# Optimization experiments

Measured on AMD Instinct MI355X. Metric: run time of the kernel, lower is better.

## Reference

```python
import jax, jax.numpy as jnp
import numpy as np

K = 32
TEMP = 0.01
OTHERWEIGHT = 0.5
BS = 64
F = 128


def setup_inputs() -> dict:
    key = jax.random.key(0)
    k1, k2, k3 = jax.random.split(key, 3)
    feats1 = jax.random.normal(k1, (K * BS, F), dtype=jnp.float32)
    feats2 = jax.random.normal(k2, (K * BS, F), dtype=jnp.float32)
    overlap_inds = jax.random.randint(k3, (K,), 0, 2).astype(bool)
    return {"feats1": feats1, "feats2": feats2, "overlap_inds": overlap_inds, "bs": BS}


def _labels(overlap_inds, bs):
    k = overlap_inds.shape[0]
    labels1 = jnp.repeat(jnp.arange(k), bs)
    nov = (~overlap_inds).astype(jnp.int32)
    excl_nov = jnp.cumsum(nov) - nov  # exclusive count of non-overlaps before i
    class2 = jnp.where(overlap_inds, jnp.arange(k), k + excl_nov)
    labels2 = jnp.repeat(class2, bs)
    return jnp.concatenate([labels1, labels2])


def reference(feats1, feats2, overlap_inds, bs):
    n1 = feats1.shape[0]
    labels = _labels(overlap_inds, bs)            # [n]
    feats = jnp.concatenate([feats1, feats2])     # [n, F]
    n = feats.shape[0]

    logits = (feats @ feats.T) * TEMP             # [n, n]; log of exp(sim*temp)
    sim = jnp.exp(logits)

    same = labels[:, None] == labels[None, :]
    eye = jnp.eye(n, dtype=bool)
    pos_mask = same & ~eye
    neg_mask = ~same

    is2 = jnp.arange(n) >= n1                     # second-view block indicator
    cross_w = jnp.where(is2[:, None] != is2[None, :], OTHERWEIGHT, 1.0)

    neg_sum = jnp.sum(jnp.where(neg_mask, sim, 0.0), axis=1)      # [n]
    # -log(pos / neg_sum) = log(neg_sum) - logits
    per_pair_loss = cross_w * (jnp.log(neg_sum)[:, None] - logits)
    total_loss = jnp.sum(jnp.where(pos_mask, per_pair_loss, 0.0))
    total_pos = jnp.sum(pos_mask)

    # accuracy: a positive pair counts iff its sim beats ALL negatives in its row
    max_neg = jnp.max(jnp.where(neg_mask, sim, -jnp.inf), axis=1)  # [n]
    correct = pos_mask & (sim > max_neg[:, None])
    acc = jnp.sum(correct).astype(jnp.float32) / total_pos.astype(jnp.float32)

    loss = total_loss / total_pos.astype(jnp.float32)
    return acc, loss
```

## Files before the change

kernel.cpp:

```cpp
#include <hip/hip_runtime.h>
#include <math.h>

#define TEMP 0.01f

typedef __attribute__((ext_vector_type(8))) short short8;
typedef __attribute__((ext_vector_type(4))) float f32x4;
typedef __attribute__((ext_vector_type(4))) unsigned short ushort4_t;


__device__ __forceinline__ unsigned bf16_hi_bits(float x) {
  unsigned u = __float_as_uint(x);
  return (u + 0x7FFFu + ((u >> 16) & 1u)) >> 16;
}

struct HL { unsigned short h, l; };

__device__ __forceinline__ HL split1(float x) {
  unsigned hb = bf16_hi_bits(x);
  float hf = __uint_as_float(hb << 16);
  unsigned lb = bf16_hi_bits(x - hf);
  HL r;
  r.h = (unsigned short)hb;
  r.l = (unsigned short)lb;
  return r;
}

__device__ __forceinline__ void decode_ov(const int* __restrict__ ov_raw,
                                          int* s_class2, int* s_v2b,
                                          int* s_ov) {
  const int t = threadIdx.x;
  if (t < 64) {
    int v = (t < 32) ? ov_raw[t] : 0;
    bool valid = (t >= 32) || (v == 0) || (v == 1);
    unsigned long long okmask = __ballot(valid);
    bool as_int = (okmask == ~0ull);
    s_v2b[t] = 0;
    if (t < 32) {
      int o = as_int ? v : (((const unsigned char*)ov_raw)[t] ? 1 : 0);
      s_ov[t] = o;
      unsigned long long nz = __ballot((t < 32) && !o);
      int cum = __popcll(nz & ((1ull << t) - 1ull));
      int c2 = o ? t : 32 + cum;
      s_class2[t] = c2;
      s_v2b[c2] = t;
    }
  }
}

__device__ __forceinline__ int labf(int g, const int* s_class2) {
  return (g < 2048) ? (g >> 6) : s_class2[(g - 2048) >> 6];
}

__global__ __launch_bounds__(256, 2) void main_kernel(
    const float* __restrict__ f1, const float* __restrict__ f2,
    const int* __restrict__ ov_raw, float* __restrict__ nsum,
    int* __restrict__ nmaxb, float* __restrict__ pcw,
    float* __restrict__ pcwl, float* __restrict__ posbuf) {
  __shared__ unsigned short Ah[128][64], Al[128][64];
  __shared__ unsigned short Bh[128][64], Bl[128][64];
  __shared__ int s_class2[32], s_v2b[64], s_ov[32];

  decode_ov(ov_raw, s_class2, s_v2b, s_ov);

  const int ibase = blockIdx.x * 128, jbase = blockIdx.y * 128;
  const float* asrc = (ibase < 2048) ? (f1 + (size_t)ibase * 128)
                                     : (f2 + (size_t)(ibase - 2048) * 128);
  const float* bsrc = (jbase < 2048) ? (f1 + (size_t)jbase * 128)
                                     : (f2 + (size_t)(jbase - 2048) * 128);
  const int t = threadIdx.x;
  const int l = t & 63;
  const int wid = t >> 6;
  const int wy = wid >> 1, wx = wid & 1;
  const int rr = l & 15;
  const int q = l >> 4;
  const int sw = l & 7;

  f32x4 acc[4][4];
#pragma unroll
  for (int mi = 0; mi < 4; ++mi)
#pragma unroll
    for (int ni = 0; ni < 4; ++ni) acc[mi][ni] = (f32x4)0.0f;

  const int kq = t & 15;
  const int r0 = t >> 4;
  const int stc = ((kq >> 1) ^ (r0 & 7)) * 8 + (kq & 1) * 4;

  for (int kc = 0; kc < 2; ++kc) {
    if (kc) __syncthreads();
#pragma unroll
    for (int p = 0; p < 8; ++p) {
      const int r = r0 + 16 * p;
      const float4 va = *(const float4*)(asrc + (size_t)r * 128 + kc * 64 + kq * 4);
      const float4 vb = *(const float4*)(bsrc + (size_t)r * 128 + kc * 64 + kq * 4);
      ushort4_t ha, la, hb, lb;
      HL s;
      s = split1(va.x); ha.x = s.h; la.x = s.l;
      s = split1(va.y); ha.y = s.h; la.y = s.l;
      s = split1(va.z); ha.z = s.h; la.z = s.l;
      s = split1(va.w); ha.w = s.h; la.w = s.l;
      s = split1(vb.x); hb.x = s.h; lb.x = s.l;
      s = split1(vb.y); hb.y = s.h; lb.y = s.l;
      s = split1(vb.z); hb.z = s.h; lb.z = s.l;
      s = split1(vb.w); hb.w = s.h; lb.w = s.l;
      *(ushort4_t*)&Ah[r][stc] = ha;
      *(ushort4_t*)&Al[r][stc] = la;
      *(ushort4_t*)&Bh[r][stc] = hb;
      *(ushort4_t*)&Bl[r][stc] = lb;
    }
    __syncthreads();

#pragma unroll
    for (int s = 0; s < 2; ++s) {
      const int pb = ((((s << 2) | q)) ^ sw) << 3;
      short8 afh[4], afl[4], bfh[4], bfl[4];
#pragma unroll
      for (int mi = 0; mi < 4; ++mi) {
        const int ar = wy * 64 + mi * 16 + rr;
        afh[mi] = *(const short8*)&Ah[ar][pb];
        afl[mi] = *(const short8*)&Al[ar][pb];
        const int br = wx * 64 + mi * 16 + rr;
        bfh[mi] = *(const short8*)&Bh[br][pb];
        bfl[mi] = *(const short8*)&Bl[br][pb];
      }
#pragma unroll
      for (int mi = 0; mi < 4; ++mi)
#pragma unroll
        for (int ni = 0; ni < 4; ++ni) {
          acc[mi][ni] = __builtin_amdgcn_mfma_f32_16x16x32_bf16(
              afh[mi], bfh[ni], acc[mi][ni], 0, 0, 0);
          acc[mi][ni] = __builtin_amdgcn_mfma_f32_16x16x32_bf16(
              afh[mi], bfl[ni], acc[mi][ni], 0, 0, 0);
          acc[mi][ni] = __builtin_amdgcn_mfma_f32_16x16x32_bf16(
              afl[mi], bfh[ni], acc[mi][ni], 0, 0, 0);
        }
    }
  }

  const float cw = ((ibase < 2048) != (jbase < 2048)) ? 0.5f : 1.0f;
  int gj[4], lj[4];
#pragma unroll
  for (int ni = 0; ni < 4; ++ni) {
    gj[ni] = jbase + wx * 64 + ni * 16 + rr;
    lj[ni] = labf(gj[ni], s_class2);
  }

#pragma unroll
  for (int mi = 0; mi < 4; ++mi) {
#pragma unroll
    for (int reg = 0; reg < 4; ++reg) {
      const int gi = ibase + wy * 64 + mi * 16 + q * 4 + reg;
      const int li = labf(gi, s_class2);
      float rnsum = 0.f, rnmax = 0.f, rpcw = 0.f, rpcwl = 0.f;
#pragma unroll
      for (int ni = 0; ni < 4; ++ni) {
        const int gjj = gj[ni];
        if (gi == gjj) continue;
        const float logit = acc[mi][ni][reg] * TEMP;
        const float e = __expf(logit);
        if (li == lj[ni]) {
          rpcw += cw;
          rpcwl += cw * logit;
          int slot;
          if (gjj < 2048) slot = gjj - (li << 6);
          else slot = ((li < 32) ? 64 : 0) + (gjj - 2048 - (s_v2b[li] << 6));
          posbuf[(size_t)gi * 128 + slot] = e;
        } else {
          rnsum += e;
          rnmax = fmaxf(rnmax, e);
        }
      }
#pragma unroll
      for (int m = 1; m < 16; m <<= 1) {
        rnsum += __shfl_xor(rnsum, m, 64);
        rpcw  += __shfl_xor(rpcw, m, 64);
        rpcwl += __shfl_xor(rpcwl, m, 64);
        rnmax = fmaxf(rnmax, __shfl_xor(rnmax, m, 64));
      }
      if (rr == 0) {
        atomicAdd(&nsum[gi], rnsum);
        atomicAdd(&pcw[gi], rpcw);
        atomicAdd(&pcwl[gi], rpcwl);
        atomicMax(&nmaxb[gi], __float_as_int(rnmax));
      }
    }
  }
}

__global__ __launch_bounds__(256) void finalize_kernel(
    const int* __restrict__ ov_raw, const float* __restrict__ nsum,
    const int* __restrict__ nmaxb, const float* __restrict__ pcw,
    const float* __restrict__ pcwl, const float* __restrict__ posbuf,
    float* __restrict__ accum, int* __restrict__ counter,
    float* __restrict__ out) {
  __shared__ int s_class2[32], s_v2b[64], s_ov[32];
  __shared__ float sc[4], sp[4], sl[4];
  decode_ov(ov_raw, s_class2, s_v2b, s_ov);
  __syncthreads();

  const int t = threadIdx.x;
  const int w = t >> 6, lane = t & 63;
  float cnt_acc = 0.f, pos_acc = 0.f, loss_acc = 0.f;
  const int rbase = blockIdx.x * 64 + w * 16;
  for (int i = 0; i < 16; ++i) {
    const int row = rbase + i;
    const float2 pv = *(const float2*)&posbuf[(size_t)row * 128 + lane * 2];
    const int c = labf(row, s_class2);
    const int size = (c < 32) ? (s_ov[c] ? 128 : 64) : 64;
    int selfslot;
    if (row < 2048) selfslot = row - (c << 6);
    else selfslot = ((c < 32) ? 64 : 0) + (row - 2048 - (s_v2b[c] << 6));
    const float nmax = __int_as_float(nmaxb[row]);
    const int s0 = lane * 2;
    int h = 0;
    if (s0 < size && s0 != selfslot && pv.x > nmax) h++;
    if (s0 + 1 < size && s0 + 1 != selfslot && pv.y > nmax) h++;
    cnt_acc += (float)h;
    if (lane == 0) {
      loss_acc += logf(nsum[row]) * pcw[row] - pcwl[row];
      pos_acc += (float)(size - 1);
    }
  }
#pragma unroll
  for (int m = 1; m < 64; m <<= 1) {
    cnt_acc += __shfl_xor(cnt_acc, m, 64);
    pos_acc += __shfl_xor(pos_acc, m, 64);
    loss_acc += __shfl_xor(loss_acc, m, 64);
  }
  if (lane == 0) { sc[w] = cnt_acc; sp[w] = pos_acc; sl[w] = loss_acc; }
  __syncthreads();
  if (t == 0) {
    atomicAdd(&accum[0], sc[0] + sc[1] + sc[2] + sc[3]);
    atomicAdd(&accum[1], sp[0] + sp[1] + sp[2] + sp[3]);
    atomicAdd(&accum[2], sl[0] + sl[1] + sl[2] + sl[3]);
    __threadfence();
    const int prev = atomicAdd(counter, 1);
    if (prev == 63) {
      const float c = atomicAdd(&accum[0], 0.0f);
      const float tp = atomicAdd(&accum[1], 0.0f);
      const float lo = atomicAdd(&accum[2], 0.0f);
      out[0] = c / tp;
      out[1] = lo / tp;
    }
  }
}

extern "C" void kernel_launch(void* const* d_in, const int* in_sizes, int n_in,
                              void* d_out, int out_size, void* d_ws,
                              size_t ws_size, hipStream_t stream) {
  const float* f1 = (const float*)d_in[0];
  const float* f2 = (const float*)d_in[1];
  const int* ov = (const int*)d_in[2];
  float* out = (float*)d_out;

  float* wsf = (float*)d_ws;
  int* wsi = (int*)d_ws;
  float* nsum   = wsf;
  int* nmaxb    = wsi + 4096;
  float* pcw    = wsf + 8192;
  float* pcwl   = wsf + 12288;
  float* accum  = wsf + 16384;
  int* counter  = wsi + 16387;
  float* posbuf = wsf + 16400;

  (void)hipMemsetAsync(nsum, 0, (size_t)16392 * sizeof(float), stream);

  dim3 grid(32, 32);
  main_kernel<<<grid, 256, 0, stream>>>(f1, f2, ov, nsum, nmaxb, pcw, pcwl,
                                        posbuf);
  finalize_kernel<<<64, 256, 0, stream>>>(ov, nsum, nmaxb, pcw, pcwl, posbuf,
                                          accum, counter, out);
}
```

Measured before the change: 110.6 us.

## Precompute bf16 hi/lo split once and stream pre-swizzled halves into tiles

Adds a precompute kernel that converts every feature row into hi/lo bf16 halves, stored in a pre-swizzled layout in workspace. The main kernel then loads these halves directly into shared memory in K-chunks of 32, instead of every tile block redoing the fp32 load and split. Using smaller LDS tiles lets it target 3 blocks per CU. The cost is an extra kernel launch, an extra global write/read pass, and a per-chunk sync loop. The old path is kept as a fallback when the workspace is too small.

```diff
diff --git a/kernel.cpp b/kernel.cpp
--- a/kernel.cpp
+++ b/kernel.cpp
@@ -6,6 +6,7 @@
 typedef __attribute__((ext_vector_type(8))) short short8;
 typedef __attribute__((ext_vector_type(4))) float f32x4;
 typedef __attribute__((ext_vector_type(4))) unsigned short ushort4_t;
+typedef __attribute__((ext_vector_type(8))) unsigned short ushort8_t;
 
 
 __device__ __forceinline__ unsigned bf16_hi_bits(float x) {
@@ -51,7 +52,157 @@
   return (g < 2048) ? (g >> 6) : s_class2[(g - 2048) >> 6];
 }
 
-__global__ __launch_bounds__(256, 2) void main_kernel(
+__global__ __launch_bounds__(256) void precompute_kernel(
+    const float* __restrict__ f1, const float* __restrict__ f2,
+    unsigned short* __restrict__ Ph, unsigned short* __restrict__ Pl) {
+  const int t = blockIdx.x * 256 + threadIdx.x;
+  const int row = t >> 4;
+  const int gid = t & 15;
+  const int gp = gid & 3, c = gid >> 2;
+  const int glog = gp ^ ((row >> 1) & 3);
+  const int k = c * 32 + glog * 8;
+  const float* src = (row < 2048) ? (f1 + (size_t)row * 128)
+                                  : (f2 + (size_t)(row - 2048) * 128);
+  const float4 a = *(const float4*)(src + k);
+  const float4 b = *(const float4*)(src + k + 4);
+  ushort8_t hi, lo;
+  HL s;
+  s = split1(a.x); hi.s0 = s.h; lo.s0 = s.l;
+  s = split1(a.y); hi.s1 = s.h; lo.s1 = s.l;
+  s = split1(a.z); hi.s2 = s.h; lo.s2 = s.l;
+  s = split1(a.w); hi.s3 = s.h; lo.s3 = s.l;
+  s = split1(b.x); hi.s4 = s.h; lo.s4 = s.l;
+  s = split1(b.y); hi.s5 = s.h; lo.s5 = s.l;
+  s = split1(b.z); hi.s6 = s.h; lo.s6 = s.l;
+  s = split1(b.w); hi.s7 = s.h; lo.s7 = s.l;
+  *(ushort8_t*)&Ph[(size_t)row * 128 + gid * 8] = hi;
+  *(ushort8_t*)&Pl[(size_t)row * 128 + gid * 8] = lo;
+}
+
+__global__ __launch_bounds__(256, 3) void main_kernel_fat(
+    const unsigned short* __restrict__ Ph, const unsigned short* __restrict__ Pl,
+    const int* __restrict__ ov_raw, float* __restrict__ nsum,
+    int* __restrict__ nmaxb, float* __restrict__ pcw,
+    float* __restrict__ pcwl, float* __restrict__ posbuf) {
+  __shared__ unsigned short Ah[128][32], Al[128][32];
+  __shared__ unsigned short Bh[128][32], Bl[128][32];
+  __shared__ int s_class2[32], s_v2b[64], s_ov[32];
+
+  decode_ov(ov_raw, s_class2, s_v2b, s_ov);
+
+  const int ibase = blockIdx.x * 128, jbase = blockIdx.y * 128;
+  const int t = threadIdx.x;
+  const int l = t & 63;
+  const int w = t >> 6;
+  const int wy = w >> 1, wx = w & 1;
+  const int rr = l & 15;
+  const int q = l >> 4;
+  const int gp = q ^ ((rr >> 1) & 3);
+
+  f32x4 acc[4][4];
+#pragma unroll
+  for (int mi = 0; mi < 4; ++mi)
+#pragma unroll
+    for (int ni = 0; ni < 4; ++ni) acc[mi][ni] = (f32x4)0.0f;
+
+  const int srow = l >> 2;
+  const int sg = l & 3;
+
+  for (int c = 0; c < 4; ++c) {
+    if (c) __syncthreads();
+    const int goff = c * 32 + sg * 8;
+#pragma unroll
+    for (int j = 0; j < 2; ++j) {
+      const int rb = w * 32 + j * 16;
+      const int r = rb + srow;
+      const size_t arec = (size_t)(ibase + r) * 128 + goff;
+      const size_t brec = (size_t)(jbase + r) * 128 + goff;
+      const ushort8_t vah = *(const ushort8_t*)&Ph[arec];
+      const ushort8_t val = *(const ushort8_t*)&Pl[arec];
+      const ushort8_t vbh = *(const ushort8_t*)&Ph[brec];
+      const ushort8_t vbl = *(const ushort8_t*)&Pl[brec];
+      *(ushort8_t*)&Ah[r][sg * 8] = vah;
+      *(ushort8_t*)&Al[r][sg * 8] = val;
+      *(ushort8_t*)&Bh[r][sg * 8] = vbh;
+      *(ushort8_t*)&Bl[r][sg * 8] = vbl;
+    }
+    __syncthreads();
+
+    short8 bfh[4], bfl[4];
+#pragma unroll
+    for (int ni = 0; ni < 4; ++ni) {
+      const int br = wx * 64 + ni * 16 + rr;
+      bfh[ni] = *(const short8*)&Bh[br][gp * 8];
+      bfl[ni] = *(const short8*)&Bl[br][gp * 8];
+    }
+#pragma unroll
+    for (int mi = 0; mi < 4; ++mi) {
+      const int ar = wy * 64 + mi * 16 + rr;
+      const short8 afh = *(const short8*)&Ah[ar][gp * 8];
+      const short8 afl = *(const short8*)&Al[ar][gp * 8];
+#pragma unroll
+      for (int ni = 0; ni < 4; ++ni) {
+        acc[mi][ni] = __builtin_amdgcn_mfma_f32_16x16x32_bf16(
+            afh, bfh[ni], acc[mi][ni], 0, 0, 0);
+        acc[mi][ni] = __builtin_amdgcn_mfma_f32_16x16x32_bf16(
+            afh, bfl[ni], acc[mi][ni], 0, 0, 0);
+        acc[mi][ni] = __builtin_amdgcn_mfma_f32_16x16x32_bf16(
+            afl, bfh[ni], acc[mi][ni], 0, 0, 0);
+      }
+    }
+  }
+
+  const float cw = ((ibase < 2048) != (jbase < 2048)) ? 0.5f : 1.0f;
+  int gj[4], lj[4];
+#pragma unroll
+  for (int ni = 0; ni < 4; ++ni) {
+    gj[ni] = jbase + wx * 64 + ni * 16 + rr;
+    lj[ni] = labf(gj[ni], s_class2);
+  }
+
+#pragma unroll
+  for (int mi = 0; mi < 4; ++mi) {
+#pragma unroll
+    for (int reg = 0; reg < 4; ++reg) {
+      const int gi = ibase + wy * 64 + mi * 16 + q * 4 + reg;
+      const int li = labf(gi, s_class2);
+      float rnsum = 0.f, rnmax = 0.f, rpcw = 0.f, rpcwl = 0.f;
+#pragma unroll
+      for (int ni = 0; ni < 4; ++ni) {
+        const int gjj = gj[ni];
+        if (gi == gjj) continue;
+        const float logit = acc[mi][ni][reg] * TEMP;
+        const float e = __expf(logit);
+        if (li == lj[ni]) {
+          rpcw += cw;
+          rpcwl += cw * logit;
+          int slot;
+          if (gjj < 2048) slot = gjj - (li << 6);
+          else slot = ((li < 32) ? 64 : 0) + (gjj - 2048 - (s_v2b[li] << 6));
+          posbuf[(size_t)gi * 128 + slot] = e;
+        } else {
+          rnsum += e;
+          rnmax = fmaxf(rnmax, e);
+        }
+      }
+#pragma unroll
+      for (int m = 1; m < 16; m <<= 1) {
+        rnsum += __shfl_xor(rnsum, m, 64);
+        rpcw  += __shfl_xor(rpcw, m, 64);
+        rpcwl += __shfl_xor(rpcwl, m, 64);
+        rnmax = fmaxf(rnmax, __shfl_xor(rnmax, m, 64));
+      }
+      if (rr == 0) {
+        atomicAdd(&nsum[gi], rnsum);
+        atomicAdd(&pcw[gi], rpcw);
+        atomicAdd(&pcwl[gi], rpcwl);
+        atomicMax(&nmaxb[gi], __float_as_int(rnmax));
+      }
+    }
+  }
+}
+
+__global__ __launch_bounds__(256, 2) void main_kernel_legacy(
     const float* __restrict__ f1, const float* __restrict__ f2,
     const int* __restrict__ ov_raw, float* __restrict__ nsum,
     int* __restrict__ nmaxb, float* __restrict__ pcw,
@@ -261,12 +412,20 @@
   float* accum  = wsf + 16384;
   int* counter  = wsi + 16387;
   float* posbuf = wsf + 16400;
+  unsigned short* Ph = (unsigned short*)(wsf + 540688);
+  unsigned short* Pl = Ph + 524288;
 
   (void)hipMemsetAsync(nsum, 0, (size_t)16392 * sizeof(float), stream);
 
   dim3 grid(32, 32);
-  main_kernel<<<grid, 256, 0, stream>>>(f1, f2, ov, nsum, nmaxb, pcw, pcwl,
-                                        posbuf);
+  if (ws_size >= (size_t)4259904) {
+    precompute_kernel<<<256, 256, 0, stream>>>(f1, f2, Ph, Pl);
+    main_kernel_fat<<<grid, 256, 0, stream>>>(Ph, Pl, ov, nsum, nmaxb, pcw,
+                                              pcwl, posbuf);
+  } else {
+    main_kernel_legacy<<<grid, 256, 0, stream>>>(f1, f2, ov, nsum, nmaxb, pcw,
+                                                 pcwl, posbuf);
+  }
   finalize_kernel<<<64, 256, 0, stream>>>(ov, nsum, nmaxb, pcw, pcwl, posbuf,
                                           accum, counter, out);
 }
```

Result: no change. 109.7 us (-0.9%).

## Exploit Gram matrix symmetry by computing only upper-triangular tiles

Applied to the files above, without the earlier changes.

Launches a 1D grid over the 528 upper-triangular 128x128 tiles and maps each block index to a (bi,bj) pair. Off-diagonal tiles additionally accumulate per-column negative sums, maxima and positive weights, and write mirrored positive entries, so the transposed tile need not be computed. This roughly halves matmul and exp work. In exchange it adds extra column shuffles, atomics and scattered posbuf stores per tile, and introduces load imbalance between diagonal and off-diagonal blocks.

```diff
diff --git a/kernel.cpp b/kernel.cpp
--- a/kernel.cpp
+++ b/kernel.cpp
@@ -51,6 +51,11 @@
   return (g < 2048) ? (g >> 6) : s_class2[(g - 2048) >> 6];
 }
 
+__device__ __forceinline__ int slotf(int g, int cls, const int* s_v2b) {
+  if (g < 2048) return g - (cls << 6);
+  return ((cls < 32) ? 64 : 0) + (g - 2048 - (s_v2b[cls] << 6));
+}
+
 __global__ __launch_bounds__(256, 2) void main_kernel(
     const float* __restrict__ f1, const float* __restrict__ f2,
     const int* __restrict__ ov_raw, float* __restrict__ nsum,
@@ -62,7 +67,14 @@
 
   decode_ov(ov_raw, s_class2, s_v2b, s_ov);
 
-  const int ibase = blockIdx.x * 128, jbase = blockIdx.y * 128;
+  const int tt = blockIdx.x;
+  int bi = (int)(32.5f - sqrtf(1056.25f - 2.0f * (float)tt));
+  while (bi * 32 - bi * (bi - 1) / 2 > tt) --bi;
+  while ((bi + 1) * 32 - (bi + 1) * bi / 2 <= tt) ++bi;
+  const int bj = bi + (tt - (bi * 32 - bi * (bi - 1) / 2));
+  const bool off = (bi != bj);
+
+  const int ibase = bi * 128, jbase = bj * 128;
   const float* asrc = (ibase < 2048) ? (f1 + (size_t)ibase * 128)
                                      : (f2 + (size_t)(ibase - 2048) * 128);
   const float* bsrc = (jbase < 2048) ? (f1 + (size_t)jbase * 128)
@@ -144,6 +156,12 @@
     lj[ni] = labf(gj[ni], s_class2);
   }
 
+  float cnsum[4], cnmax[4], cpcw[4], cpcwl[4];
+#pragma unroll
+  for (int ni = 0; ni < 4; ++ni) {
+    cnsum[ni] = 0.f; cnmax[ni] = 0.f; cpcw[ni] = 0.f; cpcwl[ni] = 0.f;
+  }
+
 #pragma unroll
   for (int mi = 0; mi < 4; ++mi) {
 #pragma unroll
@@ -160,13 +178,19 @@
         if (li == lj[ni]) {
           rpcw += cw;
           rpcwl += cw * logit;
-          int slot;
-          if (gjj < 2048) slot = gjj - (li << 6);
-          else slot = ((li < 32) ? 64 : 0) + (gjj - 2048 - (s_v2b[li] << 6));
-          posbuf[(size_t)gi * 128 + slot] = e;
+          posbuf[(size_t)gi * 128 + slotf(gjj, li, s_v2b)] = e;
+          if (off) {
+            cpcw[ni] += cw;
+            cpcwl[ni] += cw * logit;
+            posbuf[(size_t)gjj * 128 + slotf(gi, li, s_v2b)] = e;
+          }
         } else {
           rnsum += e;
           rnmax = fmaxf(rnmax, e);
+          if (off) {
+            cnsum[ni] += e;
+            cnmax[ni] = fmaxf(cnmax[ni], e);
+          }
         }
       }
 #pragma unroll
@@ -181,6 +205,27 @@
         atomicAdd(&pcw[gi], rpcw);
         atomicAdd(&pcwl[gi], rpcwl);
         atomicMax(&nmaxb[gi], __float_as_int(rnmax));
+      }
+    }
+  }
+
+  if (off) {
+#pragma unroll
+    for (int ni = 0; ni < 4; ++ni) {
+      float cs = cnsum[ni], cm = cnmax[ni], cp = cpcw[ni], cl = cpcwl[ni];
+#pragma unroll
+      for (int m = 16; m < 64; m <<= 1) {
+        cs += __shfl_xor(cs, m, 64);
+        cp += __shfl_xor(cp, m, 64);
+        cl += __shfl_xor(cl, m, 64);
+        cm = fmaxf(cm, __shfl_xor(cm, m, 64));
+      }
+      if (q == 0) {
+        const int g = gj[ni];
+        atomicAdd(&nsum[g], cs);
+        atomicAdd(&pcw[g], cp);
+        atomicAdd(&pcwl[g], cl);
+        atomicMax(&nmaxb[g], __float_as_int(cm));
       }
     }
   }
@@ -264,9 +309,8 @@
 
   (void)hipMemsetAsync(nsum, 0, (size_t)16392 * sizeof(float), stream);
 
-  dim3 grid(32, 32);
-  main_kernel<<<grid, 256, 0, stream>>>(f1, f2, ov, nsum, nmaxb, pcw, pcwl,
-                                        posbuf);
+  main_kernel<<<528, 256, 0, stream>>>(f1, f2, ov, nsum, nmaxb, pcw, pcwl,
+                                       posbuf);
   finalize_kernel<<<64, 256, 0, stream>>>(ov, nsum, nmaxb, pcw, pcwl, posbuf,
                                           accum, counter, out);
 }
```

Measured after the change: 108.1 us. -2.3%, faster.
